# Optimization experiments

Measured on AMD Instinct MI355X. Metric: run time of the kernel, lower is better.

## Reference

```python
import jax, jax.numpy as jnp
import numpy as np

B = 36          # fixed batch_size in source
T = 60          # time_window
DECAY = 0.3     # LIAF default decay
THRESH = 0.5    # LIAF default firing threshold


def conv3x3(x, W, b):
    # x: [B,C,H,W], W: [O,C,3,3], padding=1, stride=1
    y = jax.lax.conv_general_dilated(x, W, (1, 1), [(1, 1), (1, 1)],
                                     dimension_numbers=('NCHW', 'OIHW', 'NCHW'))
    return y + b[None, :, None, None]


def avgpool2(x):
    # 2x2 average pool, stride 2
    b, c, h, w = x.shape
    return x.reshape(b, c, h // 2, 2, w // 2, 2).mean(axis=(3, 5))


def liaf(u, spike, mem):
    # leaky-integrate with spike-gated reset, analog (ReLU) fire
    mem = mem * DECAY * (1.0 - spike) + u
    new_spike = (mem > THRESH).astype(mem.dtype)
    out = jax.nn.relu(mem)
    return new_spike, mem, out


def setup_inputs() -> dict:
    key = jax.random.key(0)
    ks = jax.random.split(key, 8)
    # DVS event frames in [0,3) so the >1 binarization keeps ~2/3 of pixels
    data = (jax.random.uniform(ks[0], (B, 2, 32, 32, T)) * 3.0).astype(jnp.float32)

    def w(k, shape, fan_in):
        return (jax.random.normal(k, shape) * (1.0 / np.sqrt(fan_in))).astype(jnp.float32)

    return dict(
        data=data,
        win=T,
        W0=w(ks[1], (64, 2, 3, 3), 2 * 9), b0=jnp.zeros((64,), jnp.float32),
        W1=w(ks[2], (128, 64, 3, 3), 64 * 9), b1=jnp.zeros((128,), jnp.float32),
        W2=w(ks[3], (128, 128, 3, 3), 128 * 9), b2=jnp.zeros((128,), jnp.float32),
        Wf1=w(ks[4], (256, 8192), 8192), bf1=jnp.zeros((256,), jnp.float32),
        Wf2=w(ks[5], (11, 256), 256), bf2=jnp.zeros((11,), jnp.float32),
    )


def reference(data, W0, b0, W1, b1, W2, b2, Wf1, bf1, Wf2, bf2, win):
    dtype = data.dtype
    z = lambda s: jnp.zeros(s, dtype)
    # (spike, mem) pairs for every LIAF cell + output-spike accumulator
    state0 = (
        (z((B, 64, 32, 32)), z((B, 64, 32, 32))),   # c0
        (z((B, 128, 32, 32)), z((B, 128, 32, 32))), # c1
        (z((B, 128, 16, 16)), z((B, 128, 16, 16))), # p1
        (z((B, 128, 16, 16)), z((B, 128, 16, 16))), # c2
        (z((B, 128, 8, 8)), z((B, 128, 8, 8))),     # p2
        (z((B, 256)), z((B, 256))),                 # h1
        (z((B, 11)), z((B, 11))),                   # h2
        z((B, 11)),                                 # sum of analog outputs
    )
    xs = jnp.moveaxis(data, -1, 0)[:win]

    def step(st, xt):
        c0, c1, p1, c2, p2, h1, h2, acc = st
        x = (xt > 1.0).astype(dtype)  # binarize accumulated frame
        s, m, out = liaf(conv3x3(x, W0, b0), *c0); c0 = (s, m)
        s, m, out = liaf(conv3x3(out, W1, b1), *c1); c1 = (s, m)
        s, m, out = liaf(avgpool2(out), *p1); p1 = (s, m)
        s, m, out = liaf(conv3x3(out, W2, b2), *c2); c2 = (s, m)
        s, m, out = liaf(avgpool2(out), *p2); p2 = (s, m)
        out = out.reshape(B, -1)  # [B, 8*8*128]
        s, m, out = liaf(out @ Wf1.T + bf1, *h1); h1 = (s, m)
        s, m, out = liaf(out @ Wf2.T + bf2, *h2); h2 = (s, m)
        return (c0, c1, p1, c2, p2, h1, h2, acc + out), None

    st_f, _ = jax.lax.scan(step, state0, xs)
    return st_f[-1] / T
```

## Files before the change

kernel.cpp:

```cpp
#include <hip/hip_runtime.h>

#define NB 36
#define NT 60

typedef __attribute__((ext_vector_type(8))) short short8;
typedef __attribute__((ext_vector_type(4))) float f32x4;

struct Params {
  const float *data;
  const float *W0, *b0, *W1, *b1, *W2, *b2, *Wf1, *bf1, *Wf2, *bf2;
  float *xb, *w0t;
  unsigned short *w1h, *w1l, *w2h, *w2l;
  unsigned int *xhl, *p1hl;
  float *outp2, *u1s;
  float *dm0, *dm1, *dmp1, *dm2, *dmp2, *dmh1, *dmh2;
  float *acc;
  float *zbase; int zn4;
};

__device__ __forceinline__ unsigned short bf16_rne(float v){
  unsigned int bits = __float_as_uint(v);
  unsigned int r = bits + 0x7FFFu + ((bits >> 16) & 1u);
  return (unsigned short)(r >> 16);
}
__device__ __forceinline__ unsigned int bf16pack(float v){
  unsigned short h = bf16_rne(v);
  float hf = __uint_as_float((unsigned int)h << 16);
  unsigned short l = bf16_rne(v - hf);
  return (unsigned int)h | ((unsigned int)l << 16);
}
__device__ __forceinline__ void unpack8(const unsigned int* q, short8& h8, short8& l8){
  unsigned int u[8];
  *(uint4*)&u[0] = *(const uint4*)q;
  *(uint4*)&u[4] = *(const uint4*)(q+4);
  #pragma unroll
  for(int i=0;i<8;i++){
    h8[i] = (short)(u[i] & 0xffffu);
    l8[i] = (short)(u[i] >> 16);
  }
}

__global__ void __launch_bounds__(256) k_prep(Params p){
  int gt  = blockIdx.x*256 + threadIdx.x;
  int STR = gridDim.x*256;
  if(gt < NB*11) p.acc[gt] = 0.f;
  for(int i=gt; i<p.zn4; i+=STR) ((float4*)p.zbase)[i] = make_float4(0.f,0.f,0.f,0.f);
  const int PLANE = 34*34;
  for(int i=gt; i<NT*NB*2*PLANE; i+=STR){
    int t   = i / (NB*2*PLANE);
    int rem = i % (NB*2*PLANE);
    int bc  = rem / PLANE;
    int pix = rem % PLANE;
    int ph = pix/34, pw = pix%34;
    float v = 0.f;
    if(ph>=1 && ph<=32 && pw>=1 && pw<=32){
      float d = p.data[((size_t)bc*1024 + (ph-1)*32 + (pw-1))*NT + t];
      v = (d > 1.0f) ? 1.0f : 0.0f;
    }
    p.xb[i] = v;
  }
  for(int i=gt; i<2*9*64; i+=STR){
    int co=i%64, rr=i/64; p.w0t[i] = p.W0[(co*2 + rr/9)*9 + rr%9];
  }
  for(int i=gt; i<128*576; i+=STR){
    int co = i/576, k = i%576;
    int cin = k/9, dd = k%9;
    unsigned int pk = bf16pack(p.W1[(co*64+cin)*9 + dd]);
    p.w1h[i]=(unsigned short)(pk&0xffffu); p.w1l[i]=(unsigned short)(pk>>16);
  }
  for(int i=gt; i<128*1152; i+=STR){
    int co = i/1152, k = i%1152;
    int cin = k/9, dd = k%9;
    unsigned int pk = bf16pack(p.W2[(co*128+cin)*9 + dd]);
    p.w2h[i]=(unsigned short)(pk&0xffffu); p.w2l[i]=(unsigned short)(pk>>16);
  }
}

template<int Cin,int Cout,int HW,int CO,int PX,int TY,int CS>
__global__ void __launch_bounds__(HW*TY)
k_conv0(const float* __restrict__ x, const float* __restrict__ wt,
        const float* __restrict__ bias, float* __restrict__ dm,
        unsigned int* __restrict__ outhl,
        const float* __restrict__ u1s, const float* __restrict__ bf1,
        const float* __restrict__ Wf2, const float* __restrict__ bf2,
        float* __restrict__ dmh1, float* __restrict__ dmh2,
        float* __restrict__ accv, int do_fc2)
{
  const int NCOG = Cout/CO;
  const int TH   = PX*TY;
  const int NHG  = HW/TH;
  const int NH4  = CO/4;
  const int NTHL = HW*TY;
  const int PIN  = HW+2;
  const int XR   = PX+2;
  int tile = blockIdx.x;
  int tid  = threadIdx.x;

  __shared__ __align__(16) float wl[CS*9*CO];
  __shared__ float xs[256];

  if(do_fc2 && tile < NB){
    int b = tile;
    int o = tid;
    float u = bf1[o];
    const float* pu = u1s + (size_t)b*256 + o;
    #pragma unroll
    for(int s=0;s<32;s++) u += pu[(size_t)s*NB*256];
    int idx = b*256 + o;
    float mem = dmh1[idx] + u;
    float xo = mem > 0.f ? mem : 0.f;
    dmh1[idx] = (mem > 0.5f) ? 0.f : 0.3f*mem;
    xs[o] = xo;
    __syncthreads();
    int w2id = o >> 6, ln = o & 63;
    for(int oo=w2id; oo<11; oo+=4){
      const float* wr = Wf2 + oo*256;
      float s = xs[ln]*wr[ln] + xs[ln+64]*wr[ln+64]
              + xs[ln+128]*wr[ln+128] + xs[ln+192]*wr[ln+192];
      #pragma unroll
      for(int off=32; off>0; off>>=1) s += __shfl_down(s, off, 64);
      if(ln==0){
        int i2 = b*11 + oo;
        float m2 = dmh2[i2] + s + bf2[oo];
        float ov = m2 > 0.f ? m2 : 0.f;
        dmh2[i2] = (m2 > 0.5f) ? 0.f : 0.3f*m2;
        accv[i2] += ov * (1.0f/60.0f);
      }
    }
  }

  int cog = tile % NCOG;
  int hg  = (tile/NCOG) % NHG;
  int b   = tile/(NCOG*NHG);
  int w0  = tid % HW;
  int ty  = tid / HW;
  int h0  = hg*TH + ty*PX;

  float accs[PX][CO];
  #pragma unroll
  for(int p=0;p<PX;p++)
    #pragma unroll
    for(int c=0;c<CO;c++) accs[p][c]=0.f;

  for(int cs=0; cs<Cin; cs+=CS){
    __syncthreads();
    for(int j=tid; j<CS*9*CO; j+=NTHL){
      int c  = j % CO;
      int rr = j / CO;
      wl[j] = wt[(cs*9 + rr)*Cout + cog*CO + c];
    }
    __syncthreads();

    for(int lc=0; lc<CS; lc++){
      const float* xc = x + ((size_t)b*Cin + cs + lc)*PIN*PIN + (size_t)h0*PIN + w0;
      float xv[XR][3];
      #pragma unroll
      for(int r=0;r<XR;r++)
        #pragma unroll
        for(int c=0;c<3;c++) xv[r][c] = xc[(size_t)r*PIN + c];
      const float4* w4 = (const float4*)(wl + lc*9*CO);
      #pragma unroll
      for(int dh=0;dh<3;dh++){
        #pragma unroll
        for(int g=0;g<NH4;g++){
          float4 wa = w4[(dh*3+0)*NH4+g];
          float4 wb = w4[(dh*3+1)*NH4+g];
          float4 wc = w4[(dh*3+2)*NH4+g];
          const float* A  = (const float*)&wa;
          const float* Bp = (const float*)&wb;
          const float* Cp = (const float*)&wc;
          #pragma unroll
          for(int cc=0;cc<4;cc++){
            #pragma unroll
            for(int px=0;px<PX;px++)
              accs[px][g*4+cc] += A[cc]*xv[px+dh][0] + Bp[cc]*xv[px+dh][1] + Cp[cc]*xv[px+dh][2];
          }
        }
      }
    }
  }

  int co0 = cog*CO;
  #pragma unroll
  for(int co=0; co<CO; co++){
    float bsv = bias[co0+co];
    const int OS = HW + 2;
    size_t plane = (size_t)(b*Cout + co0+co)*OS*OS;
    #pragma unroll
    for(int px=0; px<PX; px++){
      size_t idx = plane + (size_t)(h0+px+1)*OS + w0 + 1;
      float mem = dm[idx] + accs[px][co] + bsv;
      float ov = mem > 0.f ? mem : 0.f;
      dm[idx]  = (mem > 0.5f) ? 0.f : 0.3f*mem;
      outhl[idx] = bf16pack(ov);
    }
  }
}

__global__ void __launch_bounds__(256, 4)
k_conv1(const unsigned int* __restrict__ xhl,
        const unsigned short* __restrict__ w1h, const unsigned short* __restrict__ w1l,
        const float* __restrict__ bias, float* __restrict__ dm,
        float* __restrict__ dmp, unsigned int* __restrict__ p1hl)
{
  __shared__ __align__(16) unsigned int ldsu[8192];
  unsigned short* Ah = (unsigned short*)ldsu;
  unsigned short* Al = (unsigned short*)(ldsu + 1280);
  unsigned int*   Xp = ldsu + 2560;

  int bid = blockIdx.x;
  int cog = bid & 1;
  int pxg = (bid>>1) & 7;
  int b   = bid >> 4;
  int tid = threadIdx.x;
  int wv  = tid >> 6, lane = tid & 63;
  int wm = wv & 1, wn = wv >> 1;
  int n = lane & 15, quad = lane >> 4;
  int r0 = pxg*4;

  f32x4 acc[2][4];
  #pragma unroll
  for(int mo=0;mo<2;mo++)
    #pragma unroll
    for(int no=0;no<4;no++) acc[mo][no] = (f32x4){0.f,0.f,0.f,0.f};

  int aco = tid >> 2;
  int aq  = tid & 3;
  const unsigned short* whp = w1h + (size_t)(cog*64 + aco)*576 + aq*8;
  const unsigned short* wlp = w1l + (size_t)(cog*64 + aco)*576 + aq*8;
  int sk  = tid >> 3;
  int pxq = tid & 7;
  int srow = pxq >> 1;
  int scol = (pxq & 1) * 16;
  int pxb  = pxq * 16;
  int skx  = sk ^ ((pxq & 3) << 3);

  uint4 wha = *(const uint4*)(whp);
  uint4 wla = *(const uint4*)(wlp);
  unsigned int tmp[16];
  {
    int cin = sk / 9;
    int dd  = sk - cin*9;
    int dh = dd/3, dw = dd - dh*3;
    const unsigned int* sx = xhl + ((size_t)(b*64 + cin)*34 + (r0 + srow + dh))*34 + scol + dw;
    #pragma unroll
    for(int i=0;i<16;i++) tmp[i] = sx[i];
  }

  for(int ch=0; ch<18; ch++){
    __syncthreads();
    *(uint4*)&Ah[aco*40 + aq*8] = wha;
    *(uint4*)&Al[aco*40 + aq*8] = wla;
    #pragma unroll
    for(int i=0;i<16;i++) Xp[(pxb+i)*44 + skx] = tmp[i];
    __syncthreads();

    if(ch+1 < 18){
      int k0n = (ch+1)*32;
      wha = *(const uint4*)(whp + k0n);
      wla = *(const uint4*)(wlp + k0n);
      int kg = k0n + sk;
      int cin = kg / 9;
      int dd  = kg - cin*9;
      int dh = dd/3, dw = dd - dh*3;
      const unsigned int* sx = xhl + ((size_t)(b*64 + cin)*34 + (r0 + srow + dh))*34 + scol + dw;
      #pragma unroll
      for(int i=0;i<16;i++) tmp[i] = sx[i];
    }

    short8 ahf[2], alf[2];
    #pragma unroll
    for(int mo=0;mo<2;mo++){
      int row = wm*32 + mo*16 + n;
      ahf[mo] = *(const short8*)&Ah[row*40 + quad*8];
      alf[mo] = *(const short8*)&Al[row*40 + quad*8];
    }
    #pragma unroll
    for(int no=0;no<4;no++){
      int prow = wn*64 + no*16 + n;
      short8 xhf, xlf;
      unpack8(&Xp[prow*44 + ((quad ^ no) & 3)*8], xhf, xlf);
      #pragma unroll
      for(int mo=0;mo<2;mo++){
        acc[mo][no] = __builtin_amdgcn_mfma_f32_16x16x32_bf16(ahf[mo], xhf, acc[mo][no],0,0,0);
        acc[mo][no] = __builtin_amdgcn_mfma_f32_16x16x32_bf16(ahf[mo], xlf, acc[mo][no],0,0,0);
        acc[mo][no] = __builtin_amdgcn_mfma_f32_16x16x32_bf16(alf[mo], xhf, acc[mo][no],0,0,0);
      }
    }
  }

  #pragma unroll
  for(int mo=0;mo<2;mo++){
    #pragma unroll
    for(int reg=0;reg<4;reg++){
      int co = cog*64 + wm*32 + mo*16 + quad*4 + reg;
      float bsv = bias[co];
      float o[4];
      #pragma unroll
      for(int no=0;no<4;no++){
        int r = r0 + wn*2 + (no>>1);
        int c = (no&1)*16 + n;
        size_t idx = (((size_t)b*128 + co)*32 + r)*32 + c;
        float mem = dm[idx] + acc[mo][no][reg] + bsv;
        o[no] = mem > 0.f ? mem : 0.f;
        dm[idx] = (mem > 0.5f) ? 0.f : 0.3f*mem;
      }
      #pragma unroll
      for(int pp=0; pp<2; pp++){
        float s = o[pp] + o[pp+2];
        s += __shfl_xor(s, 1, 64);
        if((n&1)==0){
          int pr = pxg*2 + wn;
          int pc = pp*8 + (n>>1);
          size_t pidx = (((size_t)b*128 + co)*18 + pr+1)*18 + pc+1;
          float pm = dmp[pidx] + s*0.25f;
          float pv = pm > 0.f ? pm : 0.f;
          dmp[pidx] = (pm > 0.5f) ? 0.f : 0.3f*pm;
          p1hl[pidx] = bf16pack(pv);
        }
      }
    }
  }
}

__global__ void __launch_bounds__(256, 4)
k_conv2(const unsigned int* __restrict__ xhl,
        const unsigned short* __restrict__ w2h, const unsigned short* __restrict__ w2l,
        const float* __restrict__ bias, float* __restrict__ dm,
        float* __restrict__ dmp, float* __restrict__ outp)
{
  __shared__ __align__(16) unsigned int ldsu[5376];
  unsigned short* Ah = (unsigned short*)ldsu;
  unsigned short* Al = (unsigned short*)(ldsu + 1280);
  unsigned int*   Xp = ldsu + 2560;

  int bid = blockIdx.x;
  int cog = bid & 1;
  int pxg = (bid>>1) & 3;
  int b   = bid >> 3;
  int tid = threadIdx.x;
  int wv  = tid >> 6, lane = tid & 63;
  int wm = wv & 1, wn = wv >> 1;
  int n = lane & 15, quad = lane >> 4;
  int r0 = pxg*4;

  f32x4 acc[2][2];
  #pragma unroll
  for(int mo=0;mo<2;mo++)
    #pragma unroll
    for(int no=0;no<2;no++) acc[mo][no] = (f32x4){0.f,0.f,0.f,0.f};

  int aco = tid >> 2;
  int aq  = tid & 3;
  const unsigned short* whp = w2h + (size_t)(cog*64 + aco)*1152 + aq*8;
  const unsigned short* wlp = w2l + (size_t)(cog*64 + aco)*1152 + aq*8;
  int sk  = tid >> 3;
  int pxq = tid & 7;
  int srow = pxq >> 1;
  int scol = (pxq & 1) * 8;
  int pxb  = pxq * 8;
  int skx  = sk ^ ((pxq >> 1) << 3);

  uint4 wha = *(const uint4*)(whp);
  uint4 wla = *(const uint4*)(wlp);
  unsigned int tmp[8];
  {
    int cin = sk / 9;
    int dd  = sk - cin*9;
    int dh = dd/3, dw = dd - dh*3;
    const unsigned int* sx = xhl + ((size_t)(b*128 + cin)*18 + (r0 + srow + dh))*18 + scol + dw;
    #pragma unroll
    for(int i=0;i<8;i++) tmp[i] = sx[i];
  }

  for(int ch=0; ch<36; ch++){
    __syncthreads();
    *(uint4*)&Ah[aco*40 + aq*8] = wha;
    *(uint4*)&Al[aco*40 + aq*8] = wla;
    #pragma unroll
    for(int i=0;i<8;i++) Xp[(pxb+i)*44 + skx] = tmp[i];
    __syncthreads();

    if(ch+1 < 36){
      int k0n = (ch+1)*32;
      wha = *(const uint4*)(whp + k0n);
      wla = *(const uint4*)(wlp + k0n);
      int kg = k0n + sk;
      int cin = kg / 9;
      int dd  = kg - cin*9;
      int dh = dd/3, dw = dd - dh*3;
      const unsigned int* sx = xhl + ((size_t)(b*128 + cin)*18 + (r0 + srow + dh))*18 + scol + dw;
      #pragma unroll
      for(int i=0;i<8;i++) tmp[i] = sx[i];
    }

    short8 ahf[2], alf[2];
    #pragma unroll
    for(int mo=0;mo<2;mo++){
      int row = wm*32 + mo*16 + n;
      ahf[mo] = *(const short8*)&Ah[row*40 + quad*8];
      alf[mo] = *(const short8*)&Al[row*40 + quad*8];
    }
    #pragma unroll
    for(int no=0;no<2;no++){
      int prow = wn*32 + no*16 + n;
      short8 xhf, xlf;
      unpack8(&Xp[prow*44 + ((quad ^ (wn*2 + no)) & 3)*8], xhf, xlf);
      #pragma unroll
      for(int mo=0;mo<2;mo++){
        acc[mo][no] = __builtin_amdgcn_mfma_f32_16x16x32_bf16(ahf[mo], xhf, acc[mo][no],0,0,0);
        acc[mo][no] = __builtin_amdgcn_mfma_f32_16x16x32_bf16(ahf[mo], xlf, acc[mo][no],0,0,0);
        acc[mo][no] = __builtin_amdgcn_mfma_f32_16x16x32_bf16(alf[mo], xhf, acc[mo][no],0,0,0);
      }
    }
  }

  #pragma unroll
  for(int mo=0;mo<2;mo++){
    #pragma unroll
    for(int reg=0;reg<4;reg++){
      int co = cog*64 + wm*32 + mo*16 + quad*4 + reg;
      float bsv = bias[co];
      float o[2];
      #pragma unroll
      for(int no=0;no<2;no++){
        int r = r0 + wn*2 + no;
        int c = n;
        size_t idx = (((size_t)b*128 + co)*16 + r)*16 + c;
        float mem = dm[idx] + acc[mo][no][reg] + bsv;
        o[no] = mem > 0.f ? mem : 0.f;
        dm[idx] = (mem > 0.5f) ? 0.f : 0.3f*mem;
      }
      float s = o[0] + o[1];
      s += __shfl_xor(s, 1, 64);
      if((n&1)==0){
        int pr = pxg*2 + wn;
        int pc = n>>1;
        size_t pidx = (((size_t)b*128 + co)*8 + pr)*8 + pc;
        float pm = dmp[pidx] + s*0.25f;
        outp[pidx] = pm > 0.f ? pm : 0.f;
        dmp[pidx]  = (pm > 0.5f) ? 0.f : 0.3f*pm;
      }
    }
  }
}

__global__ void __launch_bounds__(256)
k_fc1(const float* __restrict__ X, const float* __restrict__ Wf,
      float* __restrict__ u1s){
  __shared__ __align__(16) float lds[4896];
  float* Wl = lds;
  float* Xl = lds + 32*68;
  const int tid = threadIdx.x;
  int ot = blockIdx.x & 7, ks = blockIdx.x >> 3;
  int o0 = ot*32, k0 = ks*256;
  int w_id = tid >> 6, lane = tid & 63;
  int o_l = lane & 7, bg = lane >> 3;
  float acc[4][5];
  #pragma unroll
  for(int i=0;i<4;i++)
    #pragma unroll
    for(int j=0;j<5;j++) acc[i][j]=0.f;

  for(int c=0; c<4; c++){
    int kb = k0 + c*64;
    __syncthreads();
    for(int idx=tid; idx<512; idx+=256){
      int r = idx >> 4, j = idx & 15;
      *(float4*)&Wl[r*68 + j*4] = *(const float4*)&Wf[(size_t)(o0+r)*8192 + kb + j*4];
    }
    for(int idx=tid; idx<640; idx+=256){
      int r = idx >> 4, j = idx & 15;
      float4 v = make_float4(0.f,0.f,0.f,0.f);
      if(r < NB) v = *(const float4*)&X[(size_t)r*8192 + kb + j*4];
      *(float4*)&Xl[r*68 + j*4] = v;
    }
    __syncthreads();
    #pragma unroll
    for(int c4=0; c4<4; c4++){
      int g = w_id*4 + c4;
      float4 wv[4], xv[5];
      #pragma unroll
      for(int oi=0;oi<4;oi++) wv[oi] = *(const float4*)&Wl[(o_l+8*oi)*68 + g*4];
      #pragma unroll
      for(int bi=0;bi<5;bi++) xv[bi] = *(const float4*)&Xl[(bg*5+bi)*68 + g*4];
      #pragma unroll
      for(int oi=0;oi<4;oi++)
        #pragma unroll
        for(int bi=0;bi<5;bi++)
          acc[oi][bi] += wv[oi].x*xv[bi].x + wv[oi].y*xv[bi].y
                       + wv[oi].z*xv[bi].z + wv[oi].w*xv[bi].w;
    }
  }
  __syncthreads();
  if(w_id > 0){
    float* r = lds + ((w_id-1)*64 + lane)*20;
    #pragma unroll
    for(int oi=0;oi<4;oi++)
      #pragma unroll
      for(int bi=0;bi<5;bi++) r[oi*5+bi] = acc[oi][bi];
  }
  __syncthreads();
  if(w_id == 0){
    #pragma unroll
    for(int wv=0;wv<3;wv++){
      float* r = lds + (wv*64 + lane)*20;
      #pragma unroll
      for(int oi=0;oi<4;oi++)
        #pragma unroll
        for(int bi=0;bi<5;bi++) acc[oi][bi] += r[oi*5+bi];
    }
    #pragma unroll
    for(int bi=0;bi<5;bi++){
      int b = bg*5 + bi;
      if(b < NB){
        #pragma unroll
        for(int oi=0;oi<4;oi++)
          u1s[((size_t)ks*NB + b)*256 + o0 + o_l + 8*oi] = acc[oi][bi];
      }
    }
  }
}

__global__ void __launch_bounds__(256)
k_fc2(const float* __restrict__ u1s, const float* __restrict__ bf1,
      const float* __restrict__ Wf2, const float* __restrict__ bf2,
      float* __restrict__ dmh1, float* __restrict__ dmh2, float* __restrict__ acc){
  __shared__ float xs[256];
  int b = blockIdx.x;
  int o = threadIdx.x;
  float u = bf1[o];
  const float* p = u1s + (size_t)b*256 + o;
  #pragma unroll
  for(int s=0;s<32;s++) u += p[(size_t)s*NB*256];
  int idx = b*256 + o;
  float mem = dmh1[idx] + u;
  float xo = mem > 0.f ? mem : 0.f;
  dmh1[idx] = (mem > 0.5f) ? 0.f : 0.3f*mem;
  xs[o] = xo;
  __syncthreads();
  int w_id = o >> 6, lane = o & 63;
  for(int oo=w_id; oo<11; oo+=4){
    const float* wr = Wf2 + oo*256;
    float s = xs[lane]*wr[lane] + xs[lane+64]*wr[lane+64]
            + xs[lane+128]*wr[lane+128] + xs[lane+192]*wr[lane+192];
    #pragma unroll
    for(int off=32; off>0; off>>=1) s += __shfl_down(s, off, 64);
    if(lane==0){
      int i2 = b*11 + oo;
      float m2 = dmh2[i2] + s + bf2[oo];
      float ov = m2 > 0.f ? m2 : 0.f;
      dmh2[i2] = (m2 > 0.5f) ? 0.f : 0.3f*m2;
      acc[i2] += ov * (1.0f/60.0f);
    }
  }
}

extern "C" void kernel_launch(void* const* d_in, const int* in_sizes, int n_in,
                              void* d_out, int out_size, void* d_ws, size_t ws_size,
                              hipStream_t stream) {
  Params p;
  p.data = (const float*)d_in[0];
  p.W0  = (const float*)d_in[2];  p.b0  = (const float*)d_in[3];
  p.W1  = (const float*)d_in[4];  p.b1  = (const float*)d_in[5];
  p.W2  = (const float*)d_in[6];  p.b2  = (const float*)d_in[7];
  p.Wf1 = (const float*)d_in[8];  p.bf1 = (const float*)d_in[9];
  p.Wf2 = (const float*)d_in[10]; p.bf2 = (const float*)d_in[11];
  p.acc = (float*)d_out;

  float* ws = (float*)d_ws;
  const size_t S_XB    = (size_t)NT*NB*2*34*34;
  const size_t S_W0T   = 2*9*64;
  const size_t S_W1S   = 128*576/2;
  const size_t S_W2S   = 128*1152/2;
  const size_t S_XHL   = (size_t)NB*64*34*34;
  const size_t S_P1HL  = (size_t)NB*128*18*18;
  const size_t S_OP2   = (size_t)NB*128*8*8;
  const size_t S_U1S   = (size_t)32*NB*256;
  const size_t S_DM0   = (size_t)NB*64*34*34;
  const size_t S_DM1   = (size_t)NB*128*32*32;
  const size_t S_DMP1  = (size_t)NB*128*18*18;
  const size_t S_DM2   = (size_t)NB*128*16*16;
  const size_t S_DMP2  = S_OP2;
  const size_t S_OH1   = (size_t)NB*256;

  p.xb    = ws;  ws += S_XB;
  p.w0t   = ws;  ws += S_W0T;
  p.w1h   = (unsigned short*)ws;  ws += S_W1S;
  p.w1l   = (unsigned short*)ws;  ws += S_W1S;
  p.w2h   = (unsigned short*)ws;  ws += S_W2S;
  p.w2l   = (unsigned short*)ws;  ws += S_W2S;
  p.zbase = ws;
  p.xhl   = (unsigned int*)ws;    ws += S_XHL;
  p.p1hl  = (unsigned int*)ws;    ws += S_P1HL;
  p.outp2 = ws;  ws += S_OP2;
  p.u1s   = ws;  ws += S_U1S;
  p.dm0   = ws;  ws += S_DM0;
  p.dm1   = ws;  ws += S_DM1;
  p.dmp1  = ws;  ws += S_DMP1;
  p.dm2   = ws;  ws += S_DM2;
  p.dmp2  = ws;  ws += S_DMP2;
  p.dmh1  = ws;  ws += S_OH1;
  p.dmh2  = ws;  ws += (size_t)NB*11;
  p.zn4   = (int)((ws - p.zbase) / 4);

  k_prep<<<dim3(1024), dim3(256), 0, stream>>>(p);
  for(int t=0; t<NT; t++){
    const float* xt = p.xb + (size_t)t*NB*2*34*34;
    k_conv0<2,64,32,8,4,8,2><<<dim3(288), dim3(256), 0, stream>>>(
        xt, p.w0t, p.b0, p.dm0, p.xhl,
        p.u1s, p.bf1, p.Wf2, p.bf2, p.dmh1, p.dmh2, p.acc, t > 0 ? 1 : 0);
    k_conv1<<<dim3(576), dim3(256), 0, stream>>>(
        p.xhl, p.w1h, p.w1l, p.b1, p.dm1, p.dmp1, p.p1hl);
    k_conv2<<<dim3(288), dim3(256), 0, stream>>>(
        p.p1hl, p.w2h, p.w2l, p.b2, p.dm2, p.dmp2, p.outp2);
    k_fc1<<<dim3(256), dim3(256), 0, stream>>>(p.outp2, p.Wf1, p.u1s);
  }
  k_fc2<<<dim3(36), dim3(256), 0, stream>>>(p.u1s, p.bf1, p.Wf2, p.bf2,
                                            p.dmh1, p.dmh2, p.acc);
}
```

Measured before the change: 6.047 ms.

## Halve per-block pixel tiles in conv1 and conv2 to double grid size

Conv1 and conv2 now cover half as many output rows per block (2 instead of 4), so each launch uses twice as many blocks (1152 and 576) with smaller LDS footprints and fewer accumulators. The pixel-to-wave mapping, LDS swizzle and the fused avg-pool reduction are rewritten to match, including an extra shuffle in conv2. The aim is better CU occupancy on the small per-timestep launches. The cost is that each weight chunk is reloaded by twice as many blocks and fewer MFMAs run per LDS sync.

```diff
diff --git a/kernel.cpp b/kernel.cpp
--- a/kernel.cpp
+++ b/kernel.cpp
@@ -203,26 +203,26 @@
         const float* __restrict__ bias, float* __restrict__ dm,
         float* __restrict__ dmp, unsigned int* __restrict__ p1hl)
 {
-  __shared__ __align__(16) unsigned int ldsu[8192];
+  __shared__ __align__(16) unsigned int ldsu[5376];
   unsigned short* Ah = (unsigned short*)ldsu;
   unsigned short* Al = (unsigned short*)(ldsu + 1280);
   unsigned int*   Xp = ldsu + 2560;
 
   int bid = blockIdx.x;
   int cog = bid & 1;
-  int pxg = (bid>>1) & 7;
-  int b   = bid >> 4;
+  int pxg = (bid>>1) & 15;
+  int b   = bid >> 5;
   int tid = threadIdx.x;
   int wv  = tid >> 6, lane = tid & 63;
   int wm = wv & 1, wn = wv >> 1;
   int n = lane & 15, quad = lane >> 4;
-  int r0 = pxg*4;
-
-  f32x4 acc[2][4];
+  int r0 = pxg*2;
+
+  f32x4 acc[2][2];
   #pragma unroll
   for(int mo=0;mo<2;mo++)
     #pragma unroll
-    for(int no=0;no<4;no++) acc[mo][no] = (f32x4){0.f,0.f,0.f,0.f};
+    for(int no=0;no<2;no++) acc[mo][no] = (f32x4){0.f,0.f,0.f,0.f};
 
   int aco = tid >> 2;
   int aq  = tid & 3;
@@ -230,21 +230,21 @@
   const unsigned short* wlp = w1l + (size_t)(cog*64 + aco)*576 + aq*8;
   int sk  = tid >> 3;
   int pxq = tid & 7;
-  int srow = pxq >> 1;
-  int scol = (pxq & 1) * 16;
-  int pxb  = pxq * 16;
-  int skx  = sk ^ ((pxq & 3) << 3);
+  int srow = pxq >> 2;
+  int scol = (pxq & 3) * 8;
+  int rA   = pxq * 8;
+  int skx  = sk ^ (((pxq >> 1) & 3) << 3);
 
   uint4 wha = *(const uint4*)(whp);
   uint4 wla = *(const uint4*)(wlp);
-  unsigned int tmp[16];
+  unsigned int tmp[8];
   {
     int cin = sk / 9;
     int dd  = sk - cin*9;
     int dh = dd/3, dw = dd - dh*3;
     const unsigned int* sx = xhl + ((size_t)(b*64 + cin)*34 + (r0 + srow + dh))*34 + scol + dw;
     #pragma unroll
-    for(int i=0;i<16;i++) tmp[i] = sx[i];
+    for(int i=0;i<8;i++) tmp[i] = sx[i];
   }
 
   for(int ch=0; ch<18; ch++){
@@ -252,7 +252,7 @@
     *(uint4*)&Ah[aco*40 + aq*8] = wha;
     *(uint4*)&Al[aco*40 + aq*8] = wla;
     #pragma unroll
-    for(int i=0;i<16;i++) Xp[(pxb+i)*44 + skx] = tmp[i];
+    for(int i=0;i<8;i++) Xp[(rA+i)*44 + skx] = tmp[i];
     __syncthreads();
 
     if(ch+1 < 18){
@@ -265,7 +265,7 @@
       int dh = dd/3, dw = dd - dh*3;
       const unsigned int* sx = xhl + ((size_t)(b*64 + cin)*34 + (r0 + srow + dh))*34 + scol + dw;
       #pragma unroll
-      for(int i=0;i<16;i++) tmp[i] = sx[i];
+      for(int i=0;i<8;i++) tmp[i] = sx[i];
     }
 
     short8 ahf[2], alf[2];
@@ -276,10 +276,11 @@
       alf[mo] = *(const short8*)&Al[row*40 + quad*8];
     }
     #pragma unroll
-    for(int no=0;no<4;no++){
-      int prow = wn*64 + no*16 + n;
+    for(int no=0;no<2;no++){
+      int prow = no*32 + wn*16 + n;
+      int cb = ((quad ^ (no*2 + wn)) & 3) * 8;
       short8 xhf, xlf;
-      unpack8(&Xp[prow*44 + ((quad ^ no) & 3)*8], xhf, xlf);
+      unpack8(&Xp[prow*44 + cb], xhf, xlf);
       #pragma unroll
       for(int mo=0;mo<2;mo++){
         acc[mo][no] = __builtin_amdgcn_mfma_f32_16x16x32_bf16(ahf[mo], xhf, acc[mo][no],0,0,0);
@@ -295,29 +296,26 @@
     for(int reg=0;reg<4;reg++){
       int co = cog*64 + wm*32 + mo*16 + quad*4 + reg;
       float bsv = bias[co];
-      float o[4];
-      #pragma unroll
-      for(int no=0;no<4;no++){
-        int r = r0 + wn*2 + (no>>1);
-        int c = (no&1)*16 + n;
+      float o[2];
+      #pragma unroll
+      for(int no=0;no<2;no++){
+        int r = r0 + no;
+        int c = wn*16 + n;
         size_t idx = (((size_t)b*128 + co)*32 + r)*32 + c;
         float mem = dm[idx] + acc[mo][no][reg] + bsv;
         o[no] = mem > 0.f ? mem : 0.f;
         dm[idx] = (mem > 0.5f) ? 0.f : 0.3f*mem;
       }
-      #pragma unroll
-      for(int pp=0; pp<2; pp++){
-        float s = o[pp] + o[pp+2];
-        s += __shfl_xor(s, 1, 64);
-        if((n&1)==0){
-          int pr = pxg*2 + wn;
-          int pc = pp*8 + (n>>1);
-          size_t pidx = (((size_t)b*128 + co)*18 + pr+1)*18 + pc+1;
-          float pm = dmp[pidx] + s*0.25f;
-          float pv = pm > 0.f ? pm : 0.f;
-          dmp[pidx] = (pm > 0.5f) ? 0.f : 0.3f*pm;
-          p1hl[pidx] = bf16pack(pv);
-        }
+      float s = o[0] + o[1];
+      s += __shfl_xor(s, 1, 64);
+      if((n&1)==0){
+        int pr = pxg;
+        int pc = wn*8 + (n>>1);
+        size_t pidx = (((size_t)b*128 + co)*18 + pr+1)*18 + pc+1;
+        float pm = dmp[pidx] + s*0.25f;
+        float pv = pm > 0.f ? pm : 0.f;
+        dmp[pidx] = (pm > 0.5f) ? 0.f : 0.3f*pm;
+        p1hl[pidx] = bf16pack(pv);
       }
     }
   }
@@ -329,26 +327,24 @@
         const float* __restrict__ bias, float* __restrict__ dm,
         float* __restrict__ dmp, float* __restrict__ outp)
 {
-  __shared__ __align__(16) unsigned int ldsu[5376];
+  __shared__ __align__(16) unsigned int ldsu[3968];
   unsigned short* Ah = (unsigned short*)ldsu;
   unsigned short* Al = (unsigned short*)(ldsu + 1280);
   unsigned int*   Xp = ldsu + 2560;
 
   int bid = blockIdx.x;
   int cog = bid & 1;
-  int pxg = (bid>>1) & 3;
-  int b   = bid >> 3;
+  int pxg = (bid>>1) & 7;
+  int b   = bid >> 4;
   int tid = threadIdx.x;
   int wv  = tid >> 6, lane = tid & 63;
   int wm = wv & 1, wn = wv >> 1;
   int n = lane & 15, quad = lane >> 4;
-  int r0 = pxg*4;
-
-  f32x4 acc[2][2];
-  #pragma unroll
-  for(int mo=0;mo<2;mo++)
-    #pragma unroll
-    for(int no=0;no<2;no++) acc[mo][no] = (f32x4){0.f,0.f,0.f,0.f};
+  int r0 = pxg*2;
+
+  f32x4 acc2[2];
+  #pragma unroll
+  for(int mo=0;mo<2;mo++) acc2[mo] = (f32x4){0.f,0.f,0.f,0.f};
 
   int aco = tid >> 2;
   int aq  = tid & 3;
@@ -356,21 +352,21 @@
   const unsigned short* wlp = w2l + (size_t)(cog*64 + aco)*1152 + aq*8;
   int sk  = tid >> 3;
   int pxq = tid & 7;
-  int srow = pxq >> 1;
-  int scol = (pxq & 1) * 8;
-  int pxb  = pxq * 8;
-  int skx  = sk ^ ((pxq >> 1) << 3);
+  int srow = pxq >> 2;
+  int scol = (pxq & 3) * 4;
+  int rA   = pxq * 4;
+  int skx  = sk ^ ((pxq >> 2) << 3);
 
   uint4 wha = *(const uint4*)(whp);
   uint4 wla = *(const uint4*)(wlp);
-  unsigned int tmp[8];
+  unsigned int tmp[4];
   {
     int cin = sk / 9;
     int dd  = sk - cin*9;
     int dh = dd/3, dw = dd - dh*3;
     const unsigned int* sx = xhl + ((size_t)(b*128 + cin)*18 + (r0 + srow + dh))*18 + scol + dw;
     #pragma unroll
-    for(int i=0;i<8;i++) tmp[i] = sx[i];
+    for(int i=0;i<4;i++) tmp[i] = sx[i];
   }
 
   for(int ch=0; ch<36; ch++){
@@ -378,7 +374,7 @@
     *(uint4*)&Ah[aco*40 + aq*8] = wha;
     *(uint4*)&Al[aco*40 + aq*8] = wla;
     #pragma unroll
-    for(int i=0;i<8;i++) Xp[(pxb+i)*44 + skx] = tmp[i];
+    for(int i=0;i<4;i++) Xp[(rA+i)*44 + skx] = tmp[i];
     __syncthreads();
 
     if(ch+1 < 36){
@@ -391,7 +387,7 @@
       int dh = dd/3, dw = dd - dh*3;
       const unsigned int* sx = xhl + ((size_t)(b*128 + cin)*18 + (r0 + srow + dh))*18 + scol + dw;
       #pragma unroll
-      for(int i=0;i<8;i++) tmp[i] = sx[i];
+      for(int i=0;i<4;i++) tmp[i] = sx[i];
     }
 
     short8 ahf[2], alf[2];
@@ -401,16 +397,16 @@
       ahf[mo] = *(const short8*)&Ah[row*40 + quad*8];
       alf[mo] = *(const short8*)&Al[row*40 + quad*8];
     }
-    #pragma unroll
-    for(int no=0;no<2;no++){
-      int prow = wn*32 + no*16 + n;
+    {
+      int prow = (n>>3)*16 + wn*8 + (n&7);
+      int cb = ((quad ^ (n>>3)) & 3) * 8;
       short8 xhf, xlf;
-      unpack8(&Xp[prow*44 + ((quad ^ (wn*2 + no)) & 3)*8], xhf, xlf);
+      unpack8(&Xp[prow*44 + cb], xhf, xlf);
       #pragma unroll
       for(int mo=0;mo<2;mo++){
-        acc[mo][no] = __builtin_amdgcn_mfma_f32_16x16x32_bf16(ahf[mo], xhf, acc[mo][no],0,0,0);
-        acc[mo][no] = __builtin_amdgcn_mfma_f32_16x16x32_bf16(ahf[mo], xlf, acc[mo][no],0,0,0);
-        acc[mo][no] = __builtin_amdgcn_mfma_f32_16x16x32_bf16(alf[mo], xhf, acc[mo][no],0,0,0);
+        acc2[mo] = __builtin_amdgcn_mfma_f32_16x16x32_bf16(ahf[mo], xhf, acc2[mo],0,0,0);
+        acc2[mo] = __builtin_amdgcn_mfma_f32_16x16x32_bf16(ahf[mo], xlf, acc2[mo],0,0,0);
+        acc2[mo] = __builtin_amdgcn_mfma_f32_16x16x32_bf16(alf[mo], xhf, acc2[mo],0,0,0);
       }
     }
   }
@@ -421,21 +417,18 @@
     for(int reg=0;reg<4;reg++){
       int co = cog*64 + wm*32 + mo*16 + quad*4 + reg;
       float bsv = bias[co];
-      float o[2];
-      #pragma unroll
-      for(int no=0;no<2;no++){
-        int r = r0 + wn*2 + no;
-        int c = n;
-        size_t idx = (((size_t)b*128 + co)*16 + r)*16 + c;
-        float mem = dm[idx] + acc[mo][no][reg] + bsv;
-        o[no] = mem > 0.f ? mem : 0.f;
-        dm[idx] = (mem > 0.5f) ? 0.f : 0.3f*mem;
-      }
-      float s = o[0] + o[1];
+      int r = r0 + (n>>3);
+      int c = wn*8 + (n&7);
+      size_t idx = (((size_t)b*128 + co)*16 + r)*16 + c;
+      float mem = dm[idx] + acc2[mo][reg] + bsv;
+      float o = mem > 0.f ? mem : 0.f;
+      dm[idx] = (mem > 0.5f) ? 0.f : 0.3f*mem;
+      float s = o;
+      s += __shfl_xor(s, 8, 64);
       s += __shfl_xor(s, 1, 64);
-      if((n&1)==0){
-        int pr = pxg*2 + wn;
-        int pc = n>>1;
+      if((n & 9) == 0){
+        int pr = pxg;
+        int pc = wn*4 + ((n&7)>>1);
         size_t pidx = (((size_t)b*128 + co)*8 + pr)*8 + pc;
         float pm = dmp[pidx] + s*0.25f;
         outp[pidx] = pm > 0.f ? pm : 0.f;
@@ -610,9 +603,9 @@
     k_conv0<2,64,32,8,4,8,2><<<dim3(288), dim3(256), 0, stream>>>(
         xt, p.w0t, p.b0, p.dm0, p.xhl,
         p.u1s, p.bf1, p.Wf2, p.bf2, p.dmh1, p.dmh2, p.acc, t > 0 ? 1 : 0);
-    k_conv1<<<dim3(576), dim3(256), 0, stream>>>(
+    k_conv1<<<dim3(1152), dim3(256), 0, stream>>>(
         p.xhl, p.w1h, p.w1l, p.b1, p.dm1, p.dmp1, p.p1hl);
-    k_conv2<<<dim3(288), dim3(256), 0, stream>>>(
+    k_conv2<<<dim3(576), dim3(256), 0, stream>>>(
         p.p1hl, p.w2h, p.w2l, p.b2, p.dm2, p.dmp2, p.outp2);
     k_fc1<<<dim3(256), dim3(256), 0, stream>>>(p.outp2, p.Wf1, p.u1s);
   }
```

Result: faster. 5.805 ms (-4.0%).
